# Performance work log

Measured on AMD Instinct MI355X. Metric: run time of the kernel, lower is better.

The kernel has to match this reference:

```python
import jax, jax.numpy as jnp
import numpy as np

N_NODES = 100000
N_EDGES = 1600000
D_IN = 128
D_OUT = 128


def setup_inputs() -> dict:
    key = jax.random.key(0)
    k1, k2, k3 = jax.random.split(key, 3)
    input_matrix = jax.random.normal(k1, (N_NODES, D_IN), dtype=jnp.float32)
    adjacency_coo_matrix = jax.random.randint(k2, (2, N_EDGES), 0, N_NODES, dtype=jnp.int64)
    # xavier-uniform-like init for the projection weights
    limit = float(np.sqrt(6.0 / (D_IN + D_OUT)))
    W = jax.random.uniform(k3, (D_IN, D_OUT), minval=-limit, maxval=limit, dtype=jnp.float32)
    return {"input_matrix": input_matrix, "adjacency_coo_matrix": adjacency_coo_matrix, "W": W}


def reference(input_matrix, adjacency_coo_matrix, W):
    N = input_matrix.shape[0]
    # add self edges (i -> i) for every node
    self_idx = jnp.arange(N, dtype=adjacency_coo_matrix.dtype)
    src = jnp.concatenate([adjacency_coo_matrix[0], self_idx])  # segment ids (rows of output)
    nbr = jnp.concatenate([adjacency_coo_matrix[1], self_idx])  # gather indices
    # gather neighbor features: [E+N, d_in]
    neighbors = input_matrix[nbr]
    # scatter-mean over destination nodes
    summed = jax.ops.segment_sum(neighbors, src, num_segments=N)
    counts = jax.ops.segment_sum(jnp.ones((src.shape[0],), dtype=input_matrix.dtype), src, num_segments=N)
    mean = summed / counts[:, None]  # counts >= 1 thanks to self edges
    # linear projection
    return mean @ W
```

## Files before the change

### kernel.cpp

```cpp
#include <hip/hip_runtime.h>
#include <stdint.h>

#define DIM 128
#define SB 256

typedef unsigned short u16;
typedef unsigned int u32;
typedef __attribute__((ext_vector_type(8))) short short8;
typedef __attribute__((ext_vector_type(4))) float floatx4;
typedef __attribute__((ext_vector_type(2))) float nt_f32x2;

__device__ __forceinline__ u16 f2bf(float f) {
    u32 u = __float_as_uint(f);
    if ((u & 0x7fffffffu) > 0x7f800000u) return (u16)0x7fc0;
    return (u16)((u + 0x7fffu + ((u >> 16) & 1u)) >> 16);
}

__device__ __forceinline__ float2 bfu(u32 u) {
    return make_float2(__uint_as_float(u << 16), __uint_as_float(u & 0xffff0000u));
}

__global__ void __launch_bounds__(256) k_gemm_y(const float4* __restrict__ X4,
                                                const float* __restrict__ W,
                                                u16* __restrict__ Ybf,
                                                int* __restrict__ cursor, int N) {
    __shared__ __align__(16) u16 wt[DIM * 136];
    __shared__ __align__(16) u16 a_lds[4][16 * 136];
    int t = threadIdx.x;
    int g = blockIdx.x * 256 + t;
    if (g < N) cursor[g] = 0;
    for (int i = t; i < DIM * DIM; i += 256) {
        int n = i & 127, k = i >> 7;
        wt[n * 136 + k] = f2bf(W[k * DIM + n]);
    }
    __syncthreads();
    int w = t >> 6, l = t & 63;
    int q = l >> 4, c = l & 15;
    int row0 = (blockIdx.x * 4 + w) * 16;
    #pragma unroll
    for (int rep = 0; rep < 8; ++rep) {
        int chunk = rep * 64 + l;
        int r = chunk >> 5, c4 = chunk & 31;
        int row = row0 + r;
        float4 v = (row < N) ? X4[(size_t)row * 32 + c4] : make_float4(0.f, 0.f, 0.f, 0.f);
        ushort4 h;
        h.x = f2bf(v.x); h.y = f2bf(v.y); h.z = f2bf(v.z); h.w = f2bf(v.w);
        *(ushort4*)&a_lds[w][r * 136 + c4 * 4] = h;
    }
    __syncthreads();
    floatx4 acc[8] = {};
    #pragma unroll
    for (int kt = 0; kt < 4; ++kt) {
        short8 a = *(const short8*)&a_lds[w][c * 136 + kt * 32 + q * 8];
        #pragma unroll
        for (int nt = 0; nt < 8; ++nt) {
            short8 b = *(const short8*)&wt[(nt * 16 + c) * 136 + kt * 32 + q * 8];
            acc[nt] = __builtin_amdgcn_mfma_f32_16x16x32_bf16(a, b, acc[nt], 0, 0, 0);
        }
    }
    #pragma unroll
    for (int nt = 0; nt < 8; ++nt)
        #pragma unroll
        for (int r = 0; r < 4; ++r)
            a_lds[w][(q * 4 + r) * 136 + nt * 16 + c] = f2bf(acc[nt][r]);
    #pragma unroll
    for (int rep = 0; rep < 8; ++rep) {
        int chunk = rep * 64 + l;
        int r = chunk >> 5, c4 = chunk & 31;
        int row = row0 + r;
        if (row < N)
            ((ushort4*)Ybf)[(size_t)row * 32 + c4] = *(ushort4*)&a_lds[w][r * 136 + c4 * 4];
    }
}

__global__ void __launch_bounds__(256) k_scatter(const int* __restrict__ adj,
                                                 int* __restrict__ cursor,
                                                 int* __restrict__ slots,
                                                 int E, int N, int cap) {
    int r = blockIdx.x & 7;
    int sub = blockIdx.x >> 3;
    int nsub = gridDim.x >> 3;
    int lo = N / 8 * r + min(r, N % 8);
    int hi = lo + N / 8 + (r < N % 8 ? 1 : 0);
    for (int e = sub * 256 + threadIdx.x; e < E; e += nsub * 256) {
        int d = adj[e];
        if (d < lo || d >= hi) continue;
        int nb = adj[E + e];
        int c = atomicAdd(&cursor[d], 1);
        if (c < cap) slots[(size_t)d * cap + c] = ((unsigned)nb < (unsigned)N) ? nb : 0;
    }
}

__device__ __forceinline__ void agg_core(const u32* __restrict__ Yb,
                                         const int* __restrict__ lst, int deg,
                                         int wid, int lane,
                                         float2* __restrict__ out2) {
    float2 acc = bfu(Yb[(size_t)wid * 64 + lane]);
    int idx[8];
    #pragma unroll
    for (int j = 0; j < 8; ++j) {
        int t = __builtin_nontemporal_load(&lst[j]);
        idx[j] = (j < deg) ? t : 0;
    }
    for (int base = 0; base < deg; base += 8) {
        u32 v[8];
        #pragma unroll
        for (int j = 0; j < 8; ++j) v[j] = Yb[(size_t)idx[j] * 64 + lane];
        int nxt = base + 8;
        #pragma unroll
        for (int j = 0; j < 8; ++j) {
            int t = __builtin_nontemporal_load(&lst[nxt + j]);
            idx[j] = (nxt + j < deg) ? t : 0;
        }
        #pragma unroll
        for (int j = 0; j < 8; ++j)
            if (base + j < deg) { float2 t2 = bfu(v[j]); acc.x += t2.x; acc.y += t2.y; }
    }
    float inv = 1.0f / (float)(deg + 1);
    nt_f32x2 o; o.x = acc.x * inv; o.y = acc.y * inv;
    __builtin_nontemporal_store(o, (nt_f32x2*)&out2[(size_t)wid * 64 + lane]);
}

__global__ void __launch_bounds__(256) k_agg_cap(const u32* __restrict__ Yb,
                                                 const int* __restrict__ cnt,
                                                 const int* __restrict__ slots,
                                                 float2* __restrict__ out2, int N, int cap) {
    int wid = (blockIdx.x * 256 + threadIdx.x) >> 6;
    int lane = threadIdx.x & 63;
    if (wid >= N) return;
    int deg = min(cnt[wid], cap);
    agg_core(Yb, slots + (size_t)wid * cap, deg, wid, lane, out2);
}

__global__ void __launch_bounds__(256) k_agg_off(const u32* __restrict__ Yb,
                                                 const int* __restrict__ offsets,
                                                 const int* __restrict__ sorted_nbr,
                                                 float2* __restrict__ out2, int N) {
    int wid = (blockIdx.x * 256 + threadIdx.x) >> 6;
    int lane = threadIdx.x & 63;
    if (wid >= N) return;
    int beg = offsets[wid], end = offsets[wid + 1];
    agg_core(Yb, sorted_nbr + beg, end - beg, wid, lane, out2);
}

__global__ void __launch_bounds__(256) k_hist(const int* __restrict__ adj,
                                              int* __restrict__ counts, int E, int N) {
    int r = blockIdx.x & 7;
    int sub = blockIdx.x >> 3;
    int nsub = gridDim.x >> 3;
    int lo = N / 8 * r + min(r, N % 8);
    int hi = lo + N / 8 + (r < N % 8 ? 1 : 0);
    for (int e = sub * 256 + threadIdx.x; e < E; e += nsub * 256) {
        int d = adj[e];
        if (d >= lo && d < hi) atomicAdd(&counts[d], 1);
    }
}

__global__ void __launch_bounds__(SB) k_bsum(const int* __restrict__ counts,
                                             int* __restrict__ partials, int N) {
    __shared__ int lds[SB];
    int t = threadIdx.x;
    int i = blockIdx.x * SB + t;
    lds[t] = (i < N) ? counts[i] : 0;
    __syncthreads();
    for (int off = SB / 2; off > 0; off >>= 1) {
        if (t < off) lds[t] += lds[t + off];
        __syncthreads();
    }
    if (t == 0) partials[blockIdx.x] = lds[0];
}

__global__ void __launch_bounds__(1024) k_pscan(int* __restrict__ partials,
                                                int* __restrict__ offsets, int nb, int N) {
    __shared__ int lds[1024];
    int t = threadIdx.x;
    int v0 = (t < nb) ? partials[t] : 0;
    lds[t] = v0;
    __syncthreads();
    for (int off = 1; off < 1024; off <<= 1) {
        int v = (t >= off) ? lds[t - off] : 0;
        __syncthreads();
        lds[t] += v;
        __syncthreads();
    }
    if (t < nb) partials[t] = lds[t] - v0;
    if (t == 1023) offsets[N] = lds[1023];
}

__global__ void __launch_bounds__(SB) k_scan_final(const int* __restrict__ counts_in,
                                                   const int* __restrict__ partials,
                                                   int* __restrict__ offsets,
                                                   int* __restrict__ cursor, int N) {
    __shared__ int lds[SB];
    int t = threadIdx.x;
    int i = blockIdx.x * SB + t;
    int c = (i < N) ? counts_in[i] : 0;
    lds[t] = c;
    __syncthreads();
    for (int off = 1; off < SB; off <<= 1) {
        int v = (t >= off) ? lds[t - off] : 0;
        __syncthreads();
        lds[t] += v;
        __syncthreads();
    }
    int excl = lds[t] - c + partials[blockIdx.x];
    if (i < N) {
        offsets[i] = excl;
        cursor[i] = excl;
    }
}

__global__ void __launch_bounds__(256) k_reorder(const int* __restrict__ adj,
                                                 int* __restrict__ cursor,
                                                 int* __restrict__ sorted_nbr, int E, int N) {
    int r = blockIdx.x & 7;
    int sub = blockIdx.x >> 3;
    int nsub = gridDim.x >> 3;
    int lo = N / 8 * r + min(r, N % 8);
    int hi = lo + N / 8 + (r < N % 8 ? 1 : 0);
    for (int e = sub * 256 + threadIdx.x; e < E; e += nsub * 256) {
        int d = adj[e];
        if (d < lo || d >= hi) continue;
        int nb = adj[E + e];
        int pos = atomicAdd(&cursor[d], 1);
        sorted_nbr[pos] = ((unsigned)nb < (unsigned)N) ? nb : 0;
    }
}

extern "C" void kernel_launch(void* const* d_in, const int* in_sizes, int n_in,
                              void* d_out, int out_size, void* d_ws, size_t ws_size,
                              hipStream_t stream) {
    int N = in_sizes[0] / DIM;
    int E = in_sizes[1] / 2;
    const float* X = (const float*)d_in[0];
    const int* adj = (const int*)d_in[1];
    const float* W = (const float*)d_in[2];
    float* out = (float*)d_out;

    int gemm_blocks = (N + 63) / 64;
    size_t cur_b = (size_t)N * 4;
    size_t y_b   = (size_t)N * DIM * 2;

    int cap = 0;
    if (ws_size >= cur_b + (size_t)N * 64 * 4 + y_b + 64) cap = 64;
    else if (ws_size >= cur_b + (size_t)N * 48 * 4 + y_b + 64) cap = 48;

    if (cap) {
        int* cursor = (int*)d_ws;
        int* slots  = cursor + N;
        u16* Ybf    = (u16*)(slots + (size_t)N * cap);

        k_gemm_y<<<gemm_blocks, 256, 0, stream>>>((const float4*)X, W, Ybf, cursor, N);
        k_scatter<<<2048, 256, 0, stream>>>(adj, cursor, slots, E, N, cap);
        k_agg_cap<<<(N + 3) / 4, 256, 0, stream>>>((const u32*)Ybf, cursor, slots,
                                                   (float2*)out, N, cap);
    } else {
        int nb = (N + SB - 1) / SB;
        int* cursor     = (int*)d_ws;
        int* offsets    = cursor + N;
        int* sorted_nbr = offsets + (N + 1);
        int* partials   = sorted_nbr + E;
        u16* Ybf        = (u16*)(partials + 512);

        k_gemm_y<<<gemm_blocks, 256, 0, stream>>>((const float4*)X, W, Ybf, cursor, N);
        k_hist<<<1024, 256, 0, stream>>>(adj, cursor, E, N);
        k_bsum<<<nb, SB, 0, stream>>>(cursor, partials, N);
        k_pscan<<<1, 1024, 0, stream>>>(partials, offsets, nb, N);
        k_scan_final<<<nb, SB, 0, stream>>>(cursor, partials, offsets, cursor, N);
        k_reorder<<<1024, 256, 0, stream>>>(adj, cursor, sorted_nbr, E, N);
        k_agg_off<<<(N + 3) / 4, 256, 0, stream>>>((const u32*)Ybf, offsets, sorted_nbr,
                                                   (float2*)out, N);
    }
}
```

Before: 268.1 us.

## Precompute bf16 W once, vectorize scatter reads, gather 4 neighbors per wave with uint4

```diff
diff --git a/kernel.cpp b/kernel.cpp
--- a/kernel.cpp
+++ b/kernel.cpp
@@ -8,7 +8,7 @@
 typedef unsigned int u32;
 typedef __attribute__((ext_vector_type(8))) short short8;
 typedef __attribute__((ext_vector_type(4))) float floatx4;
-typedef __attribute__((ext_vector_type(2))) float nt_f32x2;
+typedef __attribute__((ext_vector_type(4))) float nt_f32x4;
 
 __device__ __forceinline__ u16 f2bf(float f) {
     u32 u = __float_as_uint(f);
@@ -16,12 +16,20 @@
     return (u16)((u + 0x7fffu + ((u >> 16) & 1u)) >> 16);
 }
 
-__device__ __forceinline__ float2 bfu(u32 u) {
-    return make_float2(__uint_as_float(u << 16), __uint_as_float(u & 0xffff0000u));
+__global__ void __launch_bounds__(256) k_wprep(const float* __restrict__ W,
+                                               u16* __restrict__ Wbf,
+                                               u16* __restrict__ Yzero) {
+    int g = blockIdx.x * 256 + threadIdx.x;
+    if (g < DIM * DIM) {
+        int n = g >> 7, k = g & 127;
+        Wbf[g] = f2bf(W[k * DIM + n]);
+    }
+    if (blockIdx.x == 0 && threadIdx.x < 32)
+        ((ushort4*)Yzero)[threadIdx.x] = make_ushort4(0, 0, 0, 0);
 }
 
 __global__ void __launch_bounds__(256) k_gemm_y(const float4* __restrict__ X4,
-                                                const float* __restrict__ W,
+                                                const u16* __restrict__ Wbf,
                                                 u16* __restrict__ Ybf,
                                                 int* __restrict__ cursor, int N) {
     __shared__ __align__(16) u16 wt[DIM * 136];
@@ -29,9 +37,9 @@
     int t = threadIdx.x;
     int g = blockIdx.x * 256 + t;
     if (g < N) cursor[g] = 0;
-    for (int i = t; i < DIM * DIM; i += 256) {
-        int n = i & 127, k = i >> 7;
-        wt[n * 136 + k] = f2bf(W[k * DIM + n]);
+    for (int i = t; i < DIM * 16; i += 256) {
+        int row = i >> 4, c8 = i & 15;
+        *(short8*)&wt[row * 136 + c8 * 8] = *(const short8*)&Wbf[row * 128 + c8 * 8];
     }
     __syncthreads();
     int w = t >> 6, l = t & 63;
@@ -82,65 +90,102 @@
     int nsub = gridDim.x >> 3;
     int lo = N / 8 * r + min(r, N % 8);
     int hi = lo + N / 8 + (r < N % 8 ? 1 : 0);
-    for (int e = sub * 256 + threadIdx.x; e < E; e += nsub * 256) {
+    const int4* src4 = (const int4*)adj;
+    int nquad = E >> 2;
+    for (int qq = sub * 256 + threadIdx.x; qq < nquad; qq += nsub * 256) {
+        int4 s = src4[qq];
+        int e0 = qq * 4;
+        #pragma unroll
+        for (int k = 0; k < 4; ++k) {
+            int d = (k == 0) ? s.x : (k == 1) ? s.y : (k == 2) ? s.z : s.w;
+            if (d < lo || d >= hi) continue;
+            int nb = adj[E + e0 + k];
+            int c = atomicAdd(&cursor[d], 1);
+            if (c < cap) slots[(size_t)d * cap + c] = ((unsigned)nb < (unsigned)N) ? nb : 0;
+        }
+    }
+    if (sub == 0 && threadIdx.x < (E & 3)) {
+        int e = (E & ~3) + threadIdx.x;
         int d = adj[e];
-        if (d < lo || d >= hi) continue;
-        int nb = adj[E + e];
-        int c = atomicAdd(&cursor[d], 1);
-        if (c < cap) slots[(size_t)d * cap + c] = ((unsigned)nb < (unsigned)N) ? nb : 0;
-    }
-}
-
-__device__ __forceinline__ void agg_core(const u32* __restrict__ Yb,
+        if (d >= lo && d < hi) {
+            int nb = adj[E + e];
+            int c = atomicAdd(&cursor[d], 1);
+            if (c < cap) slots[(size_t)d * cap + c] = ((unsigned)nb < (unsigned)N) ? nb : 0;
+        }
+    }
+}
+
+__device__ __forceinline__ void agg_core(const uint4* __restrict__ Yb4,
                                          const int* __restrict__ lst, int deg,
-                                         int wid, int lane,
-                                         float2* __restrict__ out2) {
-    float2 acc = bfu(Yb[(size_t)wid * 64 + lane]);
-    int idx[8];
+                                         int wid, int grp, int sl, int N,
+                                         float4* __restrict__ out4) {
+    float acc[8];
+    {
+        int id0 = (grp == 0) ? wid : N;
+        uint4 v = Yb4[(size_t)id0 * 16 + sl];
+        u32 c0[4] = {v.x, v.y, v.z, v.w};
+        #pragma unroll
+        for (int k2 = 0; k2 < 4; ++k2) {
+            acc[2 * k2]     = __uint_as_float(c0[k2] << 16);
+            acc[2 * k2 + 1] = __uint_as_float(c0[k2] & 0xffff0000u);
+        }
+    }
+    for (int base = 0; base < deg; base += 16) {
+        int id[4];
+        #pragma unroll
+        for (int qi = 0; qi < 4; ++qi) {
+            int ee = base + qi * 4 + grp;
+            int t = __builtin_nontemporal_load(&lst[ee]);
+            id[qi] = (ee < deg) ? t : N;
+        }
+        uint4 v[4];
+        #pragma unroll
+        for (int qi = 0; qi < 4; ++qi)
+            v[qi] = Yb4[(size_t)id[qi] * 16 + sl];
+        #pragma unroll
+        for (int qi = 0; qi < 4; ++qi) {
+            u32 c0[4] = {v[qi].x, v[qi].y, v[qi].z, v[qi].w};
+            #pragma unroll
+            for (int k2 = 0; k2 < 4; ++k2) {
+                acc[2 * k2]     += __uint_as_float(c0[k2] << 16);
+                acc[2 * k2 + 1] += __uint_as_float(c0[k2] & 0xffff0000u);
+            }
+        }
+    }
     #pragma unroll
     for (int j = 0; j < 8; ++j) {
-        int t = __builtin_nontemporal_load(&lst[j]);
-        idx[j] = (j < deg) ? t : 0;
-    }
-    for (int base = 0; base < deg; base += 8) {
-        u32 v[8];
-        #pragma unroll
-        for (int j = 0; j < 8; ++j) v[j] = Yb[(size_t)idx[j] * 64 + lane];
-        int nxt = base + 8;
-        #pragma unroll
-        for (int j = 0; j < 8; ++j) {
-            int t = __builtin_nontemporal_load(&lst[nxt + j]);
-            idx[j] = (nxt + j < deg) ? t : 0;
-        }
-        #pragma unroll
-        for (int j = 0; j < 8; ++j)
-            if (base + j < deg) { float2 t2 = bfu(v[j]); acc.x += t2.x; acc.y += t2.y; }
+        acc[j] += __shfl_xor(acc[j], 16);
+        acc[j] += __shfl_xor(acc[j], 32);
     }
     float inv = 1.0f / (float)(deg + 1);
-    nt_f32x2 o; o.x = acc.x * inv; o.y = acc.y * inv;
-    __builtin_nontemporal_store(o, (nt_f32x2*)&out2[(size_t)wid * 64 + lane]);
-}
-
-__global__ void __launch_bounds__(256) k_agg_cap(const u32* __restrict__ Yb,
+    if (grp < 2) {
+        nt_f32x4 o;
+        o.x = acc[grp * 4 + 0] * inv; o.y = acc[grp * 4 + 1] * inv;
+        o.z = acc[grp * 4 + 2] * inv; o.w = acc[grp * 4 + 3] * inv;
+        __builtin_nontemporal_store(o, (nt_f32x4*)&out4[(size_t)wid * 32 + sl * 2 + grp]);
+    }
+}
+
+__global__ void __launch_bounds__(256) k_agg_cap(const uint4* __restrict__ Yb4,
                                                  const int* __restrict__ cnt,
                                                  const int* __restrict__ slots,
-                                                 float2* __restrict__ out2, int N, int cap) {
+                                                 float4* __restrict__ out4, int N, int cap) {
     int wid = (blockIdx.x * 256 + threadIdx.x) >> 6;
     int lane = threadIdx.x & 63;
     if (wid >= N) return;
     int deg = min(cnt[wid], cap);
-    agg_core(Yb, slots + (size_t)wid * cap, deg, wid, lane, out2);
-}
-
-__global__ void __launch_bounds__(256) k_agg_off(const u32* __restrict__ Yb,
+    agg_core(Yb4, slots + (size_t)wid * cap, deg, wid, lane >> 4, lane & 15, N, out4);
+}
+
+__global__ void __launch_bounds__(256) k_agg_off(const uint4* __restrict__ Yb4,
                                                  const int* __restrict__ offsets,
                                                  const int* __restrict__ sorted_nbr,
-                                                 float2* __restrict__ out2, int N) {
+                                                 float4* __restrict__ out4, int N) {
     int wid = (blockIdx.x * 256 + threadIdx.x) >> 6;
     int lane = threadIdx.x & 63;
     if (wid >= N) return;
     int beg = offsets[wid], end = offsets[wid + 1];
-    agg_core(Yb, sorted_nbr + beg, end - beg, wid, lane, out2);
+    agg_core(Yb4, sorted_nbr + beg, end - beg, wid, lane >> 4, lane & 15, N, out4);
 }
 
 __global__ void __launch_bounds__(256) k_hist(const int* __restrict__ adj,
@@ -238,22 +283,25 @@
     float* out = (float*)d_out;
 
     int gemm_blocks = (N + 63) / 64;
-    size_t cur_b = (size_t)N * 4;
-    size_t y_b   = (size_t)N * DIM * 2;
+    size_t cur_b  = (size_t)N * 4;
+    size_t y_b    = ((size_t)N + 1) * DIM * 2;
+    size_t wbf_b  = (size_t)DIM * DIM * 2;
 
     int cap = 0;
-    if (ws_size >= cur_b + (size_t)N * 64 * 4 + y_b + 64) cap = 64;
-    else if (ws_size >= cur_b + (size_t)N * 48 * 4 + y_b + 64) cap = 48;
+    if (ws_size >= cur_b + (size_t)N * 64 * 4 + y_b + wbf_b) cap = 64;
+    else if (ws_size >= cur_b + (size_t)N * 48 * 4 + y_b + wbf_b) cap = 48;
 
     if (cap) {
         int* cursor = (int*)d_ws;
         int* slots  = cursor + N;
         u16* Ybf    = (u16*)(slots + (size_t)N * cap);
-
-        k_gemm_y<<<gemm_blocks, 256, 0, stream>>>((const float4*)X, W, Ybf, cursor, N);
+        u16* Wbf    = Ybf + ((size_t)N + 1) * DIM;
+
+        k_wprep<<<64, 256, 0, stream>>>(W, Wbf, Ybf + (size_t)N * DIM);
+        k_gemm_y<<<gemm_blocks, 256, 0, stream>>>((const float4*)X, Wbf, Ybf, cursor, N);
         k_scatter<<<2048, 256, 0, stream>>>(adj, cursor, slots, E, N, cap);
-        k_agg_cap<<<(N + 3) / 4, 256, 0, stream>>>((const u32*)Ybf, cursor, slots,
-                                                   (float2*)out, N, cap);
+        k_agg_cap<<<(N + 3) / 4, 256, 0, stream>>>((const uint4*)Ybf, cursor, slots,
+                                                   (float4*)out, N, cap);
     } else {
         int nb = (N + SB - 1) / SB;
         int* cursor     = (int*)d_ws;
@@ -261,14 +309,16 @@
         int* sorted_nbr = offsets + (N + 1);
         int* partials   = sorted_nbr + E;
         u16* Ybf        = (u16*)(partials + 512);
-
-        k_gemm_y<<<gemm_blocks, 256, 0, stream>>>((const float4*)X, W, Ybf, cursor, N);
+        u16* Wbf        = Ybf + ((size_t)N + 1) * DIM;
+
+        k_wprep<<<64, 256, 0, stream>>>(W, Wbf, Ybf + (size_t)N * DIM);
+        k_gemm_y<<<gemm_blocks, 256, 0, stream>>>((const float4*)X, Wbf, Ybf, cursor, N);
         k_hist<<<1024, 256, 0, stream>>>(adj, cursor, E, N);
         k_bsum<<<nb, SB, 0, stream>>>(cursor, partials, N);
         k_pscan<<<1, 1024, 0, stream>>>(partials, offsets, nb, N);
         k_scan_final<<<nb, SB, 0, stream>>>(cursor, partials, offsets, cursor, N);
         k_reorder<<<1024, 256, 0, stream>>>(adj, cursor, sorted_nbr, E, N);
-        k_agg_off<<<(N + 3) / 4, 256, 0, stream>>>((const u32*)Ybf, offsets, sorted_nbr,
-                                                   (float2*)out, N);
-    }
-}
+        k_agg_off<<<(N + 3) / 4, 256, 0, stream>>>((const uint4*)Ybf, offsets, sorted_nbr,
+                                                   (float4*)out, N);
+    }
+}
```

After: 249.2 us. -7.1%, faster.
